# Kernel tuning notes

Measured on AMD Instinct MI355X. Metric: run time of the kernel, lower is better.

## Reference

```python
import jax, jax.numpy as jnp
import numpy as np
from jax import lax

B, CIN, HF, WF = 8, 512, 60, 60      # encoder feature
NCLS = 19                            # seg out channels
PATCH = 10                           # patch_size
DEPTH = 8                            # 2**att_depth
UPS = 8                              # seg upsampling
HI = HF * UPS                        # 480 upsampled image size
NP_IMG = (HI // PATCH) ** 2          # 2304 image patches
NP_FEA = (HI // DEPTH // PATCH) ** 2 # 36 feature patches
POOL_SIZES = (1, 2, 3, 6)


def resize_ac(x, H, W):
    # bilinear, align_corners=True (matches F.interpolate/UpsamplingBilinear2d)
    b, c, h, w = x.shape
    ys = jnp.arange(H, dtype=x.dtype) * ((h - 1) / max(H - 1, 1))
    xs = jnp.arange(W, dtype=x.dtype) * ((w - 1) / max(W - 1, 1))
    y0 = jnp.floor(ys).astype(jnp.int32); y1 = jnp.minimum(y0 + 1, h - 1)
    x0 = jnp.floor(xs).astype(jnp.int32); x1 = jnp.minimum(x0 + 1, w - 1)
    wy = (ys - y0.astype(x.dtype))[:, None]
    wx = (xs - x0.astype(x.dtype))[None, :]
    g = lambda yi, xi: x[:, :, yi[:, None], xi[None, :]]
    top = (1 - wx) * g(y0, x0) + wx * g(y0, x1)
    bot = (1 - wx) * g(y1, x0) + wx * g(y1, x1)
    return (1 - wy) * top + wy * bot


def bn_eval(x, gamma, beta, mean, var, eps=1e-5):
    s = lambda v: v[None, :, None, None]
    return (x - s(mean)) * (s(gamma) / jnp.sqrt(s(var) + eps)) + s(beta)


def setup_inputs() -> dict:
    key = jax.random.key(0)
    ks = jax.random.split(key, 16)
    f32 = jnp.float32
    return {
        "feat": jax.random.normal(ks[0], (B, CIN, HF, WF), f32),
        "attentions": jax.random.normal(ks[1], (B, NCLS, NP_IMG, NP_FEA), f32),
        "w_psp": jax.random.normal(ks[2], (4, CIN // 4, CIN), f32) * 0.03,
        "b_psp0": jax.random.normal(ks[3], (CIN // 4,), f32) * 0.02,
        "bn_psp_gamma": jax.random.uniform(ks[4], (3, CIN // 4), f32, 0.5, 1.5),
        "bn_psp_beta": jax.random.normal(ks[5], (3, CIN // 4), f32) * 0.02,
        "bn_psp_mean": jax.random.normal(ks[6], (3, CIN // 4), f32) * 0.02,
        "bn_psp_var": jax.random.uniform(ks[7], (3, CIN // 4), f32, 0.5, 1.5),
        "w_conv": jax.random.normal(ks[8], (512, 2 * CIN), f32) * 0.03,
        "bn_conv_gamma": jax.random.uniform(ks[9], (512,), f32, 0.5, 1.5),
        "bn_conv_beta": jax.random.normal(ks[10], (512,), f32) * 0.02,
        "bn_conv_mean": jax.random.normal(ks[11], (512,), f32) * 0.02,
        "bn_conv_var": jax.random.uniform(ks[12], (512,), f32, 0.5, 1.5),
        "w_segconv": jax.random.normal(ks[13], (NCLS, 512, 3, 3), f32) * 0.03,
        "b_segconv": jax.random.normal(ks[14], (NCLS,), f32) * 0.02,
    }


def _forward(feat, attentions, w_psp, b_psp0, bn_psp_gamma, bn_psp_beta,
             bn_psp_mean, bn_psp_var, w_conv, bn_conv_gamma, bn_conv_beta,
             bn_conv_mean, bn_conv_var, w_segconv, b_segconv):
    # ---- PSP pyramid ----
    branches = []
    for i, p in enumerate(POOL_SIZES):
        k = HF // p
        pooled = feat.reshape(B, CIN, p, k, p, k).mean(axis=(3, 5))  # adaptive avg pool
        y = jnp.einsum('oc,bchw->bohw', w_psp[i], pooled)
        if i == 0:  # pool_size==1 -> no BN, conv has bias
            y = y + b_psp0[None, :, None, None]
        else:
            y = bn_eval(y, bn_psp_gamma[i-1], bn_psp_beta[i-1],
                        bn_psp_mean[i-1], bn_psp_var[i-1])
        y = jax.nn.relu(y)
        branches.append(resize_ac(y, HF, WF))
    x = jnp.concatenate(branches + [feat], axis=1)  # [B, 2*CIN, HF, WF]

    # ---- 1x1 Conv2dReLU + BN (eval), dropout is identity in eval ----
    x = jnp.einsum('oc,bchw->bohw', w_conv, x)
    x = jax.nn.relu(bn_eval(x, bn_conv_gamma, bn_conv_beta, bn_conv_mean, bn_conv_var))

    # ---- SegmentationHead ----
    x = lax.conv_general_dilated(x, w_segconv, (1, 1), 'SAME',
                                 dimension_numbers=('NCHW', 'OIHW', 'NCHW'))
    x = x + b_segconv[None, :, None, None]
    x = resize_ac(x, HI, HI)  # [B, NCLS, 480, 480]

    # one-hot of per-pixel argmax (scatter of ones)
    am = jnp.argmax(x, axis=1)
    x_softmax = (am[:, None] == jnp.arange(NCLS)[None, :, None, None]).astype(x.dtype)

    # grouped ones-conv stride 8 / 64 == 8x8 average pooling
    hf = HI // DEPTH  # 60
    argx_feamap = x_softmax.reshape(B, NCLS, hf, DEPTH, hf, DEPTH).mean(axis=(3, 5))

    # unfold(k=10, s=10): [B, C, 36, 100] (blocks row-major, patch row-major)
    nb = hf // PATCH  # 6
    unf = argx_feamap.reshape(B, NCLS, nb, PATCH, nb, PATCH)
    unf = unf.transpose(0, 1, 2, 4, 3, 5).reshape(B, NCLS, nb * nb, PATCH * PATCH)

    counts = jnp.count_nonzero(attentions, axis=-1, keepdims=True).astype(x.dtype) + 1e-5
    att = jnp.einsum('bcpk,bckq->bcpq', attentions / counts, unf)  # [B,C,2304,100]

    # fold back to [B, C, 480, 480]
    nbi = HI // PATCH  # 48
    corr = att.reshape(B, NCLS, nbi, nbi, PATCH, PATCH)
    corr = corr.transpose(0, 1, 2, 4, 3, 5).reshape(B, NCLS, HI, HI)

    x = corr * x + x  # activation=None -> identity
    return x, attentions


def reference(feat, attentions, w_psp, b_psp0, bn_psp_gamma, bn_psp_beta,
              bn_psp_mean, bn_psp_var, w_conv, bn_conv_gamma, bn_conv_beta,
              bn_conv_mean, bn_conv_var, w_segconv, b_segconv):
    return _forward(feat, attentions, w_psp, b_psp0, bn_psp_gamma, bn_psp_beta,
                    bn_psp_mean, bn_psp_var, w_conv, bn_conv_gamma, bn_conv_beta,
                    bn_conv_mean, bn_conv_var, w_segconv, b_segconv)
```

## Files before the change

### kernel.cpp

```cpp
#include <hip/hip_runtime.h>
#include <stdint.h>

#define NB 8
#define NCLS 19

typedef short s8v __attribute__((ext_vector_type(8)));
typedef float f4v __attribute__((ext_vector_type(4)));

__device__ __forceinline__ unsigned short f2b(float f){
  union { float f; uint32_t u; } v; v.f = f;
  uint32_t u = v.u;
  uint32_t r = (u + 0x7fffu + ((u >> 16) & 1u)) >> 16;
  return (unsigned short)r;
}

#define OFF_X512 0
#define OFF_POOL 31490048
#define OFF_Z    32309248
#define OFF_BNS  33128448
#define OFF_BNB  33130496
#define OFF_SEG  33132544
#define OFF_ARGX 35321344
#define OFF_WSEG 37510144

__global__ void k_halo(unsigned short* __restrict__ x512p){
  int idx = blockIdx.x*256 + threadIdx.x;
  if (idx >= 124928) return;
  int pix = idx >> 6;
  int ch  = (idx & 63) << 3;
  int b = pix / 244;
  int r = pix - b*244;
  int h, w;
  if (r < 62){ h = 0; w = r; }
  else if (r < 124){ h = 61; w = r - 62; }
  else if (r < 184){ h = r - 124 + 1; w = 0; }
  else { h = r - 184 + 1; w = 61; }
  s8v z = (s8v){0,0,0,0,0,0,0,0};
  *(s8v*)(x512p + (((size_t)b*62 + h)*62 + w)*512 + ch) = z;
}

__global__ void k0_copy(const float4* __restrict__ in, float4* __restrict__ out, int n4){
  for (int i = blockIdx.x*blockDim.x + threadIdx.x; i < n4; i += gridDim.x*blockDim.x)
    out[i] = in[i];
}

__global__ void kprep(const float* __restrict__ wseg, unsigned short* __restrict__ wsegT){
  int idx = blockIdx.x*256 + threadIdx.x;
  if (idx >= 9*32*512) return;
  int tap = idx / (32*512);
  int rem = idx - tap*(32*512);
  int o = rem >> 9, c = rem & 511;
  float v = (o < NCLS) ? wseg[((size_t)o*512 + c)*9 + tap] : 0.0f;
  wsegT[idx] = f2b(v);
}

__global__ void kbn(const float* __restrict__ g, const float* __restrict__ be,
                    const float* __restrict__ m, const float* __restrict__ v,
                    float* __restrict__ sc, float* __restrict__ sh){
  int i = blockIdx.x*256 + threadIdx.x;
  if (i < 512){
    float s = g[i] * rsqrtf(v[i] + 1e-5f);
    sc[i] = s; sh[i] = be[i] - m[i]*s;
  }
}

__global__ __launch_bounds__(64) void k1_pool(const float* __restrict__ feat, float* __restrict__ pooled){
  int bc = blockIdx.x;
  __shared__ float rs[64][12];
  int r = threadIdx.x;
  if (r < 60){
    const float* row = feat + (size_t)bc*3600 + r*60;
    float s6[6];
    #pragma unroll
    for (int j = 0; j < 6; j++){
      float s = 0.f;
      #pragma unroll
      for (int i = 0; i < 10; i++) s += row[j*10+i];
      s6[j] = s;
    }
    float s3_0 = s6[0]+s6[1], s3_1 = s6[2]+s6[3], s3_2 = s6[4]+s6[5];
    float s2_0 = s3_0 + s6[2], s2_1 = s6[3] + s3_2;
    rs[r][0]  = s2_0 + s2_1;
    rs[r][1]  = s2_0; rs[r][2]  = s2_1;
    rs[r][3]  = s3_0; rs[r][4]  = s3_1; rs[r][5] = s3_2;
    #pragma unroll
    for (int j = 0; j < 6; j++) rs[r][6+j] = s6[j];
  }
  __syncthreads();
  int t = threadIdx.x;
  if (t < 50){
    int P, by, bx, jcol;
    if (t == 0){ P=1; by=0; bx=0; jcol=0; }
    else if (t < 5){ P=2; int l=t-1; by=l>>1; bx=l&1; jcol=1+bx; }
    else if (t < 14){ P=3; int l=t-5; by=l/3; bx=l-(l/3)*3; jcol=3+bx; }
    else { P=6; int l=t-14; by=l/6; bx=l-(l/6)*6; jcol=6+bx; }
    int k = 60/P;
    float s = 0.f;
    for (int rr = 0; rr < k; rr++) s += rs[by*k+rr][jcol];
    pooled[(size_t)bc*50 + t] = s * (1.0f/((float)k*(float)k));
  }
}

__global__ __launch_bounds__(256) void k2_branch(
    const float* __restrict__ pooled, const float* __restrict__ w_psp,
    const float* __restrict__ b_psp0,
    const float* __restrict__ png, const float* __restrict__ pnb,
    const float* __restrict__ pnm, const float* __restrict__ pnv,
    const float* __restrict__ wconv, float* __restrict__ zbuf)
{
  int bin = blockIdx.x % 50;
  int b   = blockIdx.x / 50;
  int br  = (bin < 1) ? 0 : (bin < 5) ? 1 : (bin < 14) ? 2 : 3;
  __shared__ float pl[512];
  __shared__ float ysh[128];
  int t = threadIdx.x;
  pl[t]       = pooled[((size_t)b*512 + t)*50 + bin];
  pl[t + 256] = pooled[((size_t)b*512 + t + 256)*50 + bin];
  __syncthreads();
  if (t < 128){
    const float* wr = w_psp + ((size_t)br*128 + t)*512;
    float s = 0.f;
    #pragma unroll 8
    for (int c = 0; c < 512; c++) s += pl[c]*wr[c];
    if (br == 0) s += b_psp0[t];
    else {
      int ib = (br-1)*128 + t;
      s = (s - pnm[ib]) * png[ib] * rsqrtf(pnv[ib] + 1e-5f) + pnb[ib];
    }
    ysh[t] = fmaxf(s, 0.f);
  }
  __syncthreads();
  for (int o = t; o < 512; o += 256){
    const float* wc = wconv + (size_t)o*1024 + br*128;
    float s = 0.f;
    #pragma unroll
    for (int c = 0; c < 128; c++) s += ysh[c]*wc[c];
    zbuf[((size_t)b*50 + bin)*512 + o] = s;
  }
}

__global__ __launch_bounds__(256) void k3_gemm(
    const float* __restrict__ feat, const float* __restrict__ wconv,
    const float* __restrict__ zbuf, const float* __restrict__ bns,
    const float* __restrict__ bnb, unsigned short* __restrict__ x512p)
{
  __shared__ unsigned short lmem[2*128*64];
  unsigned short* lA = lmem;
  unsigned short* lB = lmem + 128*64;

  const int t = threadIdx.x;
  const int lane = t & 63;
  const int wave = t >> 6;
  const int wm = wave >> 1;
  const int wn = wave & 1;
  const int pix0 = blockIdx.x * 128;
  const int o0   = blockIdx.y * 128;
  const int b    = blockIdx.z;

  f4v acc[4][4];
  #pragma unroll
  for (int i = 0; i < 4; i++)
    #pragma unroll
    for (int j = 0; j < 4; j++)
      acc[i][j] = (f4v){0.f,0.f,0.f,0.f};

  const int pA = t >> 1;
  const int hA = t & 1;
  const int pclamp = min(pix0 + pA, 3599);
  const int orow_l = t >> 4;
  const int cq = t & 15;

  for (int kk = 0; kk < 8; kk++){
    {
      const float* src = feat + ((size_t)b*512 + (size_t)(kk*64 + hA*32))*3600 + pclamp;
      #pragma unroll
      for (int j = 0; j < 4; j++){
        s8v v;
        #pragma unroll
        for (int e = 0; e < 8; e++)
          v[e] = (short)f2b(src[(size_t)(j*8+e)*3600]);
        int cn = hA*4 + j;
        *(s8v*)((char*)lA + pA*128 + ((cn ^ (pA & 7)))*16) = v;
      }
    }
    {
      #pragma unroll
      for (int rr = 0; rr < 8; rr++){
        int o = rr*16 + orow_l;
        float4 wv = *(const float4*)(wconv + (size_t)(o0 + o)*1024 + 512 + kk*64 + cq*4);
        ushort4 pv;
        pv.x = f2b(wv.x); pv.y = f2b(wv.y); pv.z = f2b(wv.z); pv.w = f2b(wv.w);
        int slot = (cq >> 1) ^ (o & 7);
        *(ushort4*)((char*)lB + o*128 + slot*16 + (cq & 1)*8) = pv;
      }
    }
    __syncthreads();
    #pragma unroll
    for (int ks = 0; ks < 2; ks++){
      const int chunk = ks*4 + (lane >> 4);
      s8v af[4], bg[4];
      #pragma unroll
      for (int mf = 0; mf < 4; mf++){
        int p = wm*64 + mf*16 + (lane & 15);
        af[mf] = *(s8v*)((char*)lA + p*128 + ((chunk ^ (p & 7)))*16);
      }
      #pragma unroll
      for (int nf = 0; nf < 4; nf++){
        int o = wn*64 + nf*16 + (lane & 15);
        bg[nf] = *(s8v*)((char*)lB + o*128 + ((chunk ^ (o & 7)))*16);
      }
      #pragma unroll
      for (int mf = 0; mf < 4; mf++)
        #pragma unroll
        for (int nf = 0; nf < 4; nf++)
          acc[mf][nf] = __builtin_amdgcn_mfma_f32_16x16x32_bf16(af[mf], bg[nf], acc[mf][nf], 0, 0, 0);
    }
    __syncthreads();
  }

  float* zl  = (float*)lmem;
  float* lsc = zl + 50*128;
  float* lsh = lsc + 128;
  for (int i = t; i < 50*128; i += 256){
    int bin = i >> 7, ol = i & 127;
    zl[i] = zbuf[((size_t)b*50 + bin)*512 + o0 + ol];
  }
  if (t < 128){ lsc[t] = bns[o0 + t]; lsh[t] = bnb[o0 + t]; }
  __syncthreads();

  #pragma unroll
  for (int mf = 0; mf < 4; mf++){
    #pragma unroll
    for (int r = 0; r < 4; r++){
      int p = pix0 + wm*64 + mf*16 + (lane >> 4)*4 + r;
      if (p >= 3600) continue;
      int h = p / 60, w = p - (p/60)*60;
      float wgt[3][4]; int bix[3][4];
      const int pbase[3] = {1,5,14};
      const int psz[3]   = {2,3,6};
      #pragma unroll
      for (int ib = 0; ib < 3; ib++){
        int P = psz[ib];
        float fy = (float)h * (float)(P-1) / 59.0f;
        float fx = (float)w * (float)(P-1) / 59.0f;
        int y0 = (int)fy; int y1 = min(y0+1, P-1); float wy = fy - (float)y0;
        int x0 = (int)fx; int x1 = min(x0+1, P-1); float wx = fx - (float)x0;
        bix[ib][0] = pbase[ib] + y0*P + x0; wgt[ib][0] = (1.f-wy)*(1.f-wx);
        bix[ib][1] = pbase[ib] + y0*P + x1; wgt[ib][1] = (1.f-wy)*wx;
        bix[ib][2] = pbase[ib] + y1*P + x0; wgt[ib][2] = wy*(1.f-wx);
        bix[ib][3] = pbase[ib] + y1*P + x1; wgt[ib][3] = wy*wx;
      }
      size_t obase = (((size_t)b*62 + (h+1))*62 + (w+1))*512 + o0;
      #pragma unroll
      for (int nf = 0; nf < 4; nf++){
        int ol = wn*64 + nf*16 + (lane & 15);
        float zs = zl[ol];
        #pragma unroll
        for (int ib = 0; ib < 3; ib++)
          #pragma unroll
          for (int tp = 0; tp < 4; tp++)
            zs += wgt[ib][tp] * zl[bix[ib][tp]*128 + ol];
        float v = acc[mf][nf][r] + zs;
        v = fmaxf(v * lsc[ol] + lsh[ol], 0.f);
        x512p[obase + ol] = f2b(v);
      }
    }
  }
}

__global__ __launch_bounds__(256) void k4_conv(
    const unsigned short* __restrict__ x512p, const unsigned short* __restrict__ wsegT,
    const float* __restrict__ bseg, float* __restrict__ seg60)
{
  __shared__ unsigned short lW[32*512];
  const int h = blockIdx.x;
  const int b = blockIdx.y;
  const int t = threadIdx.x;
  const int lane = t & 63;
  const int wave = t >> 6;
  const int wpix = wave*16 + (lane & 15);
  const int wld = min(wpix, 59);

  f4v acc[2];
  acc[0] = (f4v){0.f,0.f,0.f,0.f};
  acc[1] = (f4v){0.f,0.f,0.f,0.f};

  for (int tap = 0; tap < 9; tap++){
    __syncthreads();
    for (int i = t; i < 2048; i += 256){
      int orow = i >> 6;
      int cn = i & 63;
      s8v v = *(const s8v*)(wsegT + ((size_t)tap*32 + orow)*512 + cn*8);
      *(s8v*)((char*)lW + orow*1024 + ((cn ^ (orow & 7)))*16) = v;
    }
    __syncthreads();
    int dy = tap/3 - 1, dx = tap - (tap/3)*3 - 1;
    const unsigned short* arow = x512p + (((size_t)b*62 + (h+dy+1))*62 + (wld+dx+1))*512 + (lane>>4)*8;
    #pragma unroll 4
    for (int cs = 0; cs < 16; cs++){
      int cb = cs*32;
      s8v a = *(const s8v*)(arow + cb);
      #pragma unroll
      for (int nf = 0; nf < 2; nf++){
        int o = nf*16 + (lane & 15);
        int chunk = (cb >> 3) + (lane >> 4);
        s8v bv = *(s8v*)((char*)lW + o*1024 + ((chunk ^ (o & 7)))*16);
        acc[nf] = __builtin_amdgcn_mfma_f32_16x16x32_bf16(a, bv, acc[nf], 0, 0, 0);
      }
    }
  }
  #pragma unroll
  for (int nf = 0; nf < 2; nf++){
    int o = nf*16 + (lane & 15);
    if (o < NCLS){
      float bias = bseg[o];
      #pragma unroll
      for (int r = 0; r < 4; r++){
        int wst = wave*16 + (lane >> 4)*4 + r;
        if (wst < 60)
          seg60[(((size_t)b*60 + h)*60 + wst)*NCLS + o] = acc[nf][r] + bias;
      }
    }
  }
}

__global__ __launch_bounds__(256) void k5_argmax(const float* __restrict__ seg60, float* __restrict__ argx){
  int gw = blockIdx.x*4 + (threadIdx.x >> 6);
  int b = gw / 3600;
  int cell = gw - b*3600;
  int fy = cell / 60, fx = cell - (cell/60)*60;
  int lane = threadIdx.x & 63;
  int py = fy*8 + (lane >> 3), px = fx*8 + (lane & 7);
  float yy = (float)py * (59.0f/479.0f); int y0 = (int)yy; int y1 = min(y0+1, 59); float wy = yy - (float)y0;
  float xx = (float)px * (59.0f/479.0f); int x0 = (int)xx; int x1 = min(x0+1, 59); float wx = xx - (float)x0;
  const float* base = seg60 + (size_t)b*3600*NCLS;
  const float* s00 = base + (y0*60 + x0)*NCLS;
  const float* s01 = base + (y0*60 + x1)*NCLS;
  const float* s10 = base + (y1*60 + x0)*NCLS;
  const float* s11 = base + (y1*60 + x1)*NCLS;
  float w00 = (1.f-wy)*(1.f-wx), w01 = (1.f-wy)*wx, w10 = wy*(1.f-wx), w11 = wy*wx;
  float best = -3.0e38f; int bc = 0;
  #pragma unroll
  for (int c = 0; c < NCLS; c++){
    float v = w00*s00[c] + w01*s01[c] + w10*s10[c] + w11*s11[c];
    if (v > best){ best = v; bc = c; }
  }
  int cnt = 0;
  #pragma unroll
  for (int c = 0; c < NCLS; c++){
    unsigned long long m = __ballot(bc == c);
    if (lane == c) cnt = __popcll(m);
  }
  int ky = fy/10, qy = fy - (fy/10)*10, kx = fx/10, qx = fx - (fx/10)*10;
  int qidx = (ky*6+kx)*100 + qy*10 + qx;
  if (lane < NCLS)
    argx[((size_t)b*NCLS + lane)*3600 + qidx] = (float)cnt * (1.0f/64.0f);
}

__global__ __launch_bounds__(256) void k7_final(
    const float* __restrict__ att, const float* __restrict__ argx,
    const float* __restrict__ seg60, float* __restrict__ out)
{
  int pr = blockIdx.x, c = blockIdx.y, b = blockIdx.z;
  __shared__ float lds[7104];
  float* latA  = lds;
  float* U     = lds + 1920;
  float* corrl = lds;
  float* hrow  = lds + 4800;
  float* inv   = lds + 6784;
  float* srow  = lds + 6832;
  const int t = threadIdx.x;

  const float* ab = att + (((size_t)b*NCLS + c)*2304 + (size_t)pr*48)*36;
  for (int i = t; i < 432; i += 256){
    int pc = i/9, j = i - pc*9;
    *(f4v*)(latA + pc*40 + j*4) = *(const f4v*)(ab + pc*36 + j*4);
  }
  const f4v* ub4 = (const f4v*)(argx + ((size_t)b*NCLS + c)*3600);
  for (int i = t; i < 900; i += 256)
    ((f4v*)U)[i] = ub4[i];
  __syncthreads();

  int ybase;
  { float yy0 = (float)(pr*10) * (59.0f/479.0f); ybase = (int)yy0; }

  f4v acc[6];
  int tp = 0, tq = 0;
  if (t < 200){
    tp = t/25; tq = t - tp*25;
    #pragma unroll
    for (int r = 0; r < 6; r++) acc[r] = (f4v){0.f,0.f,0.f,0.f};
    #pragma unroll 4
    for (int k = 0; k < 36; k++){
      f4v u = *(const f4v*)(U + k*100 + tq*4);
      #pragma unroll
      for (int r = 0; r < 6; r++)
        acc[r] += latA[(tp*6+r)*40 + k] * u;
    }
  } else {
    int idx = t - 200;
    if (idx < 48){
      int nz = 0;
      #pragma unroll
      for (int k = 0; k < 36; k++) nz += (latA[idx*40+k] != 0.f) ? 1 : 0;
      inv[idx] = 1.0f / ((float)nz + 1e-5f);
    }
    for (int i = idx; i < 240; i += 56){
      int j = i/60, x = i - (i/60)*60;
      int row = min(ybase + j, 59);
      srow[j*64 + x] = seg60[(((size_t)b*60 + row)*60 + x)*NCLS + c];
    }
  }
  __syncthreads();

  if (t < 200){
    #pragma unroll
    for (int r = 0; r < 6; r++){
      int pc = tp*6 + r;
      *(f4v*)(corrl + pc*100 + tq*4) = acc[r] * inv[pc];
    }
  }
  for (int i = t; i < 1920; i += 256){
    int j = i/480, px = i - j*480;
    float xx = (float)px * (59.0f/479.0f);
    int x0 = (int)xx; int x1 = min(x0+1, 59); float wx = xx - (float)x0;
    hrow[j*480 + px] = (1.f-wx)*srow[j*64 + x0] + wx*srow[j*64 + x1];
  }
  __syncthreads();

  float* outb = out + ((size_t)b*NCLS + c)*230400 + (size_t)pr*4800;
  for (int qy = 0; qy < 10; qy++){
    int py = pr*10 + qy;
    float yy = (float)py * (59.0f/479.0f);
    int y0 = (int)yy; int y1 = min(y0+1, 59); float wy = yy - (float)y0;
    const float* h0 = hrow + (y0 - ybase)*480;
    const float* h1 = hrow + (y1 - ybase)*480;
    float omw = 1.f - wy;
    for (int px = t; px < 480; px += 256){
      float xv = omw*h0[px] + wy*h1[px];
      int pc = (px*6554) >> 16;
      int qx = px - pc*10;
      float corr = corrl[pc*100 + qy*10 + qx];
      outb[qy*480 + px] = xv * (1.f + corr);
    }
  }
}

extern "C" void kernel_launch(void* const* d_in, const int* in_sizes, int n_in,
                              void* d_out, int out_size, void* d_ws, size_t ws_size,
                              hipStream_t stream)
{
  (void)in_sizes; (void)n_in; (void)out_size; (void)ws_size;
  const float* feat   = (const float*)d_in[0];
  const float* attn   = (const float*)d_in[1];
  const float* w_psp  = (const float*)d_in[2];
  const float* b_psp0 = (const float*)d_in[3];
  const float* png    = (const float*)d_in[4];
  const float* pnb    = (const float*)d_in[5];
  const float* pnm    = (const float*)d_in[6];
  const float* pnv    = (const float*)d_in[7];
  const float* wconv  = (const float*)d_in[8];
  const float* cg     = (const float*)d_in[9];
  const float* cbt    = (const float*)d_in[10];
  const float* cm     = (const float*)d_in[11];
  const float* cv     = (const float*)d_in[12];
  const float* wseg   = (const float*)d_in[13];
  const float* bseg   = (const float*)d_in[14];

  float* out1 = (float*)d_out;
  float* out2 = out1 + (size_t)35020800;

  char* ws = (char*)d_ws;
  unsigned short* x512p = (unsigned short*)(ws + OFF_X512);
  float* pooled = (float*)(ws + OFF_POOL);
  float* zbuf   = (float*)(ws + OFF_Z);
  float* bns    = (float*)(ws + OFF_BNS);
  float* bnb    = (float*)(ws + OFF_BNB);
  float* seg60  = (float*)(ws + OFF_SEG);
  float* argx   = (float*)(ws + OFF_ARGX);
  unsigned short* wsegT = (unsigned short*)(ws + OFF_WSEG);

  k_halo<<<488, 256, 0, stream>>>(x512p);
  kprep<<<576, 256, 0, stream>>>(wseg, wsegT);
  kbn<<<2, 256, 0, stream>>>(cg, cbt, cm, cv, bns, bnb);
  k0_copy<<<2048, 256, 0, stream>>>((const float4*)attn, (float4*)out2, 12607488/4);
  k1_pool<<<4096, 64, 0, stream>>>(feat, pooled);
  k2_branch<<<400, 256, 0, stream>>>(pooled, w_psp, b_psp0, png, pnb, pnm, pnv, wconv, zbuf);
  k3_gemm<<<dim3(29,4,8), 256, 0, stream>>>(feat, wconv, zbuf, bns, bnb, x512p);
  k4_conv<<<dim3(60,8), 256, 0, stream>>>(x512p, wsegT, bseg, seg60);
  k5_argmax<<<7200, 256, 0, stream>>>(seg60, argx);
  k7_final<<<dim3(48,19,8), 256, 0, stream>>>(attn, argx, seg60, out1);
}
```

Measured before the change: 296.3 us.

## Pretranspose feat and conv weights to bf16, load GEMM tiles via global_load_lds

Adds a transpose kernel that writes feat as pixel-major bf16 into scratch space borrowed from the output buffer, and a prep kernel that converts the conv weight half to bf16. The GEMM then fills its LDS tiles with direct 16-byte global-to-LDS loads, keeping the XOR swizzle, instead of strided fp32 loads plus in-register conversion. The attention copy is moved after the GEMM so the borrowed output region is only overwritten once featT is no longer needed. This adds two extra passes and the write traffic for the transposed copy.

```diff
diff --git a/kernel.cpp b/kernel.cpp
--- a/kernel.cpp
+++ b/kernel.cpp
@@ -13,6 +13,10 @@
   uint32_t r = (u + 0x7fffu + ((u >> 16) & 1u)) >> 16;
   return (unsigned short)r;
 }
+
+#define GLOAD16(g, l) __builtin_amdgcn_global_load_lds( \
+    (const __attribute__((address_space(1))) unsigned int*)(g), \
+    (__attribute__((address_space(3))) unsigned int*)(l), 16, 0, 0)
 
 #define OFF_X512 0
 #define OFF_POOL 31490048
@@ -22,6 +26,7 @@
 #define OFF_SEG  33132544
 #define OFF_ARGX 35321344
 #define OFF_WSEG 37510144
+#define OFF_WF   37805056
 
 __global__ void k_halo(unsigned short* __restrict__ x512p){
   int idx = blockIdx.x*256 + threadIdx.x;
@@ -52,6 +57,29 @@
   int o = rem >> 9, c = rem & 511;
   float v = (o < NCLS) ? wseg[((size_t)o*512 + c)*9 + tap] : 0.0f;
   wsegT[idx] = f2b(v);
+}
+
+__global__ void kprep2(const float* __restrict__ wconv, unsigned short* __restrict__ wfT){
+  int idx = blockIdx.x*256 + threadIdx.x;
+  if (idx >= 512*512) return;
+  int o = idx >> 9, c = idx & 511;
+  wfT[idx] = f2b(wconv[(size_t)o*1024 + 512 + c]);
+}
+
+__global__ __launch_bounds__(256) void ktr(const float* __restrict__ feat, unsigned short* __restrict__ featT){
+  __shared__ unsigned short lt[64*528];
+  int px0 = blockIdx.x*64, b = blockIdx.y;
+  for (int i = threadIdx.x; i < 64*512; i += 256){
+    int c = i >> 6, px = i & 63;
+    float v = feat[((size_t)b*512 + c)*3600 + min(px0+px, 3599)];
+    lt[px*528 + c] = f2b(v);
+  }
+  __syncthreads();
+  for (int i = threadIdx.x; i < 4096; i += 256){
+    int px = i >> 6, c8 = i & 63;
+    s8v v = *(const s8v*)(lt + px*528 + c8*8);
+    *(s8v*)(featT + ((size_t)b*3712 + px0 + px)*512 + c8*8) = v;
+  }
 }
 
 __global__ void kbn(const float* __restrict__ g, const float* __restrict__ be,
@@ -140,7 +168,7 @@
 }
 
 __global__ __launch_bounds__(256) void k3_gemm(
-    const float* __restrict__ feat, const float* __restrict__ wconv,
+    const unsigned short* __restrict__ featT, const unsigned short* __restrict__ wfT,
     const float* __restrict__ zbuf, const float* __restrict__ bns,
     const float* __restrict__ bnb, unsigned short* __restrict__ x512p)
 {
@@ -164,35 +192,22 @@
     for (int j = 0; j < 4; j++)
       acc[i][j] = (f4v){0.f,0.f,0.f,0.f};
 
-  const int pA = t >> 1;
-  const int hA = t & 1;
-  const int pclamp = min(pix0 + pA, 3599);
-  const int orow_l = t >> 4;
-  const int cq = t & 15;
+  const int sub  = lane >> 3;
+  const int slot = lane & 7;
 
   for (int kk = 0; kk < 8; kk++){
-    {
-      const float* src = feat + ((size_t)b*512 + (size_t)(kk*64 + hA*32))*3600 + pclamp;
-      #pragma unroll
-      for (int j = 0; j < 4; j++){
-        s8v v;
-        #pragma unroll
-        for (int e = 0; e < 8; e++)
-          v[e] = (short)f2b(src[(size_t)(j*8+e)*3600]);
-        int cn = hA*4 + j;
-        *(s8v*)((char*)lA + pA*128 + ((cn ^ (pA & 7)))*16) = v;
-      }
-    }
-    {
-      #pragma unroll
-      for (int rr = 0; rr < 8; rr++){
-        int o = rr*16 + orow_l;
-        float4 wv = *(const float4*)(wconv + (size_t)(o0 + o)*1024 + 512 + kk*64 + cq*4);
-        ushort4 pv;
-        pv.x = f2b(wv.x); pv.y = f2b(wv.y); pv.z = f2b(wv.z); pv.w = f2b(wv.w);
-        int slot = (cq >> 1) ^ (o & 7);
-        *(ushort4*)((char*)lB + o*128 + slot*16 + (cq & 1)*8) = pv;
-      }
+    #pragma unroll
+    for (int j = 0; j < 4; j++){
+      int px = j*32 + wave*8 + sub;
+      int pix = min(pix0 + px, 3599);
+      const unsigned short* src = featT + ((size_t)b*3712 + pix)*512 + kk*64 + ((slot ^ (px & 7)) << 3);
+      GLOAD16(src, lA + j*2048 + wave*512);
+    }
+    #pragma unroll
+    for (int j = 0; j < 4; j++){
+      int o = j*32 + wave*8 + sub;
+      const unsigned short* src = wfT + (size_t)(o0 + o)*512 + kk*64 + ((slot ^ (o & 7)) << 3);
+      GLOAD16(src, lB + j*2048 + wave*512);
     }
     __syncthreads();
     #pragma unroll
@@ -479,14 +494,18 @@
   float* seg60  = (float*)(ws + OFF_SEG);
   float* argx   = (float*)(ws + OFF_ARGX);
   unsigned short* wsegT = (unsigned short*)(ws + OFF_WSEG);
+  unsigned short* wfT   = (unsigned short*)(ws + OFF_WF);
+  unsigned short* featT = (unsigned short*)d_out;
 
   k_halo<<<488, 256, 0, stream>>>(x512p);
   kprep<<<576, 256, 0, stream>>>(wseg, wsegT);
+  kprep2<<<1024, 256, 0, stream>>>(wconv, wfT);
+  ktr<<<dim3(57,8), 256, 0, stream>>>(feat, featT);
   kbn<<<2, 256, 0, stream>>>(cg, cbt, cm, cv, bns, bnb);
-  k0_copy<<<2048, 256, 0, stream>>>((const float4*)attn, (float4*)out2, 12607488/4);
   k1_pool<<<4096, 64, 0, stream>>>(feat, pooled);
   k2_branch<<<400, 256, 0, stream>>>(pooled, w_psp, b_psp0, png, pnb, pnm, pnv, wconv, zbuf);
-  k3_gemm<<<dim3(29,4,8), 256, 0, stream>>>(feat, wconv, zbuf, bns, bnb, x512p);
+  k3_gemm<<<dim3(29,4,8), 256, 0, stream>>>(featT, wfT, zbuf, bns, bnb, x512p);
+  k0_copy<<<2048, 256, 0, stream>>>((const float4*)attn, (float4*)out2, 12607488/4);
   k4_conv<<<dim3(60,8), 256, 0, stream>>>(x512p, wsegT, bseg, seg60);
   k5_argmax<<<7200, 256, 0, stream>>>(seg60, argx);
   k7_final<<<dim3(48,19,8), 256, 0, stream>>>(attn, argx, seg60, out1);
```

Measured after the change: 300.8 us. Within noise of the previous version (+1.5%).
